# Kernel optimization log

Hardware: AMD Instinct MI355X
Metric: run time of the kernel (lower is better)

The kernel has to match this reference:

```python
import jax, jax.numpy as jnp
import numpy as np

BLOCK = 32          # MX block size along the last (contraction) dim
E4M3_MAX = 448.0    # max representable magnitude of float8_e4m3fn
E4M3_MAX_POW2 = 8.0 # floor(log2(448))


def mx_quant_dequant(x):
    """Emulate torchao MXTensor.to_mx: per-32-block shared E8M0 scale + fp8 e4m3 cast,
    then dequantize back to fp32 (what torch.matmul on MXTensor computes with)."""
    orig_shape = x.shape
    xb = x.reshape(orig_shape[:-1] + (orig_shape[-1] // BLOCK, BLOCK))
    amax = jnp.max(jnp.abs(xb), axis=-1, keepdims=True)
    safe_amax = jnp.where(amax == 0, 1.0, amax)
    # shared power-of-two exponent: floor(log2(amax)) - max_pow2(e4m3)
    shared_exp = jnp.floor(jnp.log2(safe_amax)) - E4M3_MAX_POW2
    scale = jnp.exp2(jnp.clip(shared_exp, -127.0, 127.0))  # E8M0 range
    q = jnp.clip(xb / scale, -E4M3_MAX, E4M3_MAX).astype(jnp.float8_e4m3fn)
    return (q.astype(x.dtype) * scale).reshape(orig_shape)


def setup_inputs() -> dict:
    key = jax.random.key(0)
    k1, k2, k3 = jax.random.split(key, 3)
    M = K = N = 4096
    return {
        "x_mx": jax.random.normal(k1, (M, K), dtype=jnp.float32),
        "mat1": jax.random.normal(k2, (K, K), dtype=jnp.float32),
        "mat2": jax.random.normal(k3, (K, N), dtype=jnp.float32),
    }


def reference(x_mx, mat1, mat2):
    # inputs arrive as MX tensors in the original -> quantize/dequantize them first
    xq = mx_quant_dequant(x_mx)
    m1q = mx_quant_dequant(mat1)
    m2q = mx_quant_dequant(mat2)
    x_high = xq @ m1q                       # [M, K] fp32 matmul of dequantized MX
    x_requant = mx_quant_dequant(x_high)    # re-quantize intermediate to MX fp8
    out = x_requant @ m2q                   # [M, N]
    return out
```

## Files before the change

### kernel.cpp

```cpp
#include <hip/hip_runtime.h>
#include <cstdint>

typedef unsigned short u16;
typedef __bf16 bf16x8 __attribute__((ext_vector_type(8)));
typedef float f32x4 __attribute__((ext_vector_type(4)));
typedef float f32x2 __attribute__((ext_vector_type(2)));

#define AS1 __attribute__((address_space(1)))
#define AS3 __attribute__((address_space(3)))


__device__ __forceinline__ int floor_log2(float x) {
    unsigned b = __float_as_uint(x);
    if (b < 0x00800000u) {
        b = __float_as_uint(x * 16777216.0f);
        return (int)(b >> 23) - 151;
    }
    return (int)(b >> 23) - 127;
}

__device__ __forceinline__ float exp2i(int e) {
    if (e >= -126) return __uint_as_float((unsigned)(e + 127) << 23);
    return __uint_as_float(0x00400000u >> (-127 - e));
}

__device__ __forceinline__ int shared_exp(float amax) {
    float safe = (amax == 0.0f) ? 1.0f : amax;
    int se = floor_log2(safe) - 8;
    return se < -127 ? -127 : (se > 127 ? 127 : se);
}

__device__ __forceinline__ void qdq2s(float v0, float v1, float i0, float i1,
                                      float s0, float s1, float& o0, float& o1) {
    float y0 = fminf(fmaxf(v0 * i0, -448.0f), 448.0f);
    float y1 = fminf(fmaxf(v1 * i1, -448.0f), 448.0f);
    int pk = __builtin_amdgcn_cvt_pk_fp8_f32(y0, y1, 0, false);
    f32x2 f = __builtin_amdgcn_cvt_pk_f32_fp8(pk, false);
    o0 = f.x * s0;
    o1 = f.y * s1;
}

__device__ __forceinline__ unsigned pack_bf16(float a, float b) {
    return (__float_as_uint(a) >> 16) | (__float_as_uint(b) & 0xffff0000u);
}


__device__ __forceinline__ void qdq_rows_body(const float* __restrict__ in,
                                              u16* __restrict__ out, int bid) {
    size_t t = (size_t)bid * 256 + threadIdx.x;
    float4 v0 = ((const float4*)in)[t * 2];
    float4 v1 = ((const float4*)in)[t * 2 + 1];
    float a = fmaxf(fmaxf(fabsf(v0.x), fabsf(v0.y)), fmaxf(fabsf(v0.z), fabsf(v0.w)));
    a = fmaxf(a, fmaxf(fmaxf(fabsf(v1.x), fabsf(v1.y)), fmaxf(fabsf(v1.z), fabsf(v1.w))));
    a = fmaxf(a, __shfl_xor(a, 1));
    a = fmaxf(a, __shfl_xor(a, 2));
    int se = shared_exp(a);
    float s = exp2i(se), inv = exp2i(-se);
    float q0, q1, q2, q3, q4, q5, q6, q7;
    qdq2s(v0.x, v0.y, inv, inv, s, s, q0, q1);
    qdq2s(v0.z, v0.w, inv, inv, s, s, q2, q3);
    qdq2s(v1.x, v1.y, inv, inv, s, s, q4, q5);
    qdq2s(v1.z, v1.w, inv, inv, s, s, q6, q7);
    uint4 o;
    o.x = pack_bf16(q0, q1);
    o.y = pack_bf16(q2, q3);
    o.z = pack_bf16(q4, q5);
    o.w = pack_bf16(q6, q7);
    ((uint4*)out)[t] = o;
}

__device__ __forceinline__ void qdq_transpose_body(const float* __restrict__ in,
                                                   u16* __restrict__ out,
                                                   int bx, int by,
                                                   u16 (*tile)[70]) {
    const int R = 4096, C = 4096;
    int c0 = bx * 64, r0 = by * 64;
    int t = threadIdx.x;
    #pragma unroll
    for (int p = 0; p < 4; ++p) {
        int lin = p * 256 + t;
        int row = lin >> 4;
        int c4  = lin & 15;
        float4 v = *(const float4*)(in + (size_t)(r0 + row) * C + c0 + c4 * 4);
        float a = fmaxf(fmaxf(fabsf(v.x), fabsf(v.y)), fmaxf(fabsf(v.z), fabsf(v.w)));
        a = fmaxf(a, __shfl_xor(a, 1));
        a = fmaxf(a, __shfl_xor(a, 2));
        a = fmaxf(a, __shfl_xor(a, 4));
        int se = shared_exp(a);
        float s = exp2i(se), inv = exp2i(-se);
        float q0, q1, q2, q3;
        qdq2s(v.x, v.y, inv, inv, s, s, q0, q1);
        qdq2s(v.z, v.w, inv, inv, s, s, q2, q3);
        tile[c4 * 4 + 0][row] = (u16)(__float_as_uint(q0) >> 16);
        tile[c4 * 4 + 1][row] = (u16)(__float_as_uint(q1) >> 16);
        tile[c4 * 4 + 2][row] = (u16)(__float_as_uint(q2) >> 16);
        tile[c4 * 4 + 3][row] = (u16)(__float_as_uint(q3) >> 16);
    }
    __syncthreads();
    #pragma unroll
    for (int p = 0; p < 4; ++p) {
        int lin = p * 256 + t;
        int n  = lin >> 4;
        int k4 = lin & 15;
        unsigned lo = *(const unsigned*)&tile[n][k4 * 4];
        unsigned hi = *(const unsigned*)&tile[n][k4 * 4 + 2];
        *(uint2*)(out + (size_t)(c0 + n) * R + r0 + k4 * 4) = make_uint2(lo, hi);
    }
}

__global__ void qdq_all(const float* __restrict__ x,  u16* __restrict__ xq,
                        const float* __restrict__ m1, u16* __restrict__ m1qT,
                        const float* __restrict__ m2, u16* __restrict__ m2qT) {
    __shared__ u16 tile[64][70];
    int bid = blockIdx.x;
    if (bid < 8192) {
        qdq_rows_body(x, xq, bid);
    } else if (bid < 12288) {
        int j = bid - 8192;
        qdq_transpose_body(m1, m1qT, j & 63, j >> 6, tile);
    } else {
        int j = bid - 12288;
        qdq_transpose_body(m2, m2qT, j & 63, j >> 6, tile);
    }
}

__device__ __forceinline__ void gemm_core256(const u16* __restrict__ A,
                                             const u16* __restrict__ B,
                                             u16* As, u16* Bs,
                                             int m0, int n0, f32x4 acc[8][4]) {
    const int K = 4096;
    const int t = threadIdx.x;
    const int w = t >> 6, lane = t & 63;
    const int l15 = lane & 15, lq = lane >> 4, fr = l15 & 7;
    const int wmc = (w >> 2) * 64;
    const int wnc = (w & 3) * 32;

    int aofs[2], bofs[2];
    #pragma unroll
    for (int ks = 0; ks < 2; ++ks) {
        aofs[ks] = (wmc + l15) * 64 + (((ks * 4 + lq) ^ fr) * 8);
        bofs[ks] = (wnc + l15) * 64 + (((ks * 4 + lq) ^ fr) * 8);
    }

    const int ch0 = t, ch1 = 512 + t;
    const int r0 = ch0 >> 3, r1 = ch1 >> 3;
    const size_t soff0 = (size_t)r0 * K + ((ch0 & 7) ^ (r0 & 7)) * 8;
    const size_t soff1 = (size_t)r1 * K + ((ch1 & 7) ^ (r1 & 7)) * 8;
    const int doff0 = ch0 * 8, doff1 = ch1 * 8;

    const u16* pA0 = A + (size_t)m0 * K;
    const u16* pA1 = A + (size_t)(m0 + 128) * K;
    const u16* pB0 = B + (size_t)n0 * K;
    const u16* pB1 = B + (size_t)(n0 + 128) * K;

    u16* A0b0 = As;            u16* A1b0 = As + 8192;
    u16* A0b1 = As + 16384;    u16* A1b1 = As + 24576;
    u16* B0b0 = Bs;            u16* B1b0 = Bs + 8192;
    u16* B0b1 = Bs + 16384;    u16* B1b1 = Bs + 24576;

#define STAGE(dst, src, kt) do {                                                          \
    __builtin_amdgcn_global_load_lds((const AS1 unsigned*)((src) + soff0 + (size_t)(kt) * 64), \
                                     (AS3 unsigned*)&(dst)[doff0], 16, 0, 0);             \
    __builtin_amdgcn_global_load_lds((const AS1 unsigned*)((src) + soff1 + (size_t)(kt) * 64), \
                                     (AS3 unsigned*)&(dst)[doff1], 16, 0, 0); } while (0)

#define LOAD_A(dst, base) do {                                                            \
    _Pragma("unroll") for (int m = 0; m < 4; ++m)                                         \
    _Pragma("unroll") for (int ks = 0; ks < 2; ++ks)                                      \
        dst[m][ks] = *(const bf16x8*)&(base)[aofs[ks] + m * 1024]; } while (0)

#define LOAD_B(dst, base) do {                                                            \
    _Pragma("unroll") for (int nf = 0; nf < 2; ++nf)                                      \
    _Pragma("unroll") for (int ks = 0; ks < 2; ++ks)                                      \
        dst[nf][ks] = *(const bf16x8*)&(base)[bofs[ks] + nf * 1024]; } while (0)

#define MFMA_Q(mb, nb, AF, BF) do {                                                       \
    _Pragma("unroll") for (int ks = 0; ks < 2; ++ks)                                      \
    _Pragma("unroll") for (int m = 0; m < 4; ++m)                                         \
    _Pragma("unroll") for (int nf = 0; nf < 2; ++nf)                                      \
        acc[(mb) + m][(nb) + nf] = __builtin_amdgcn_mfma_f32_16x16x32_bf16(               \
            AF[m][ks], BF[nf][ks], acc[(mb) + m][(nb) + nf], 0, 0, 0); } while (0)

#define MID() do { __builtin_amdgcn_s_barrier();                                          \
    asm volatile("s_waitcnt lgkmcnt(0)" ::: "memory");                                    \
    __builtin_amdgcn_s_setprio(1); } while (0)
#define END() do { __builtin_amdgcn_s_setprio(0); __builtin_amdgcn_s_barrier(); } while (0)
#define VMW() asm volatile("s_waitcnt vmcnt(6)" ::: "memory")

    #pragma unroll
    for (int mi = 0; mi < 8; ++mi)
        #pragma unroll
        for (int ni = 0; ni < 4; ++ni)
            acc[mi][ni] = (f32x4)0.f;

    bf16x8 afA[4][2], afB[4][2], bf0[2][2], bf1[2][2];

    STAGE(A0b0, pA0, 0);
    STAGE(B1b0, pB1, 0);
    STAGE(A1b0, pA1, 0);
    STAGE(B0b0, pB0, 0);
    STAGE(A0b1, pA0, 1);
    STAGE(B1b1, pB1, 1);
    STAGE(A1b1, pA1, 1);
    VMW();
    __builtin_amdgcn_s_barrier();
    LOAD_A(afA, A0b0); LOAD_B(bf0, B0b0);

    #pragma unroll 1
    for (int i = 0; i < 32; ++i) {
        const int t1 = (2 * i + 1) & 63, t2 = (2 * i + 2) & 63, t3 = (2 * i + 3) & 63;
        STAGE(B0b1, pB0, t1);
        MID(); LOAD_B(bf1, B1b0); MFMA_Q(0, 0, afA, bf0); END();
        STAGE(A0b0, pA0, t2);
        MID(); LOAD_A(afB, A1b0); MFMA_Q(0, 2, afA, bf1); END();
        STAGE(B1b0, pB1, t2);
        MID(); MFMA_Q(4, 2, afB, bf1); END();
        STAGE(A1b0, pA1, t2);
        VMW();
        MID(); LOAD_A(afA, A0b1); LOAD_B(bf1, B0b1); MFMA_Q(4, 0, afB, bf0); END();
        STAGE(B0b0, pB0, t2);
        MID(); LOAD_B(bf0, B1b1); MFMA_Q(0, 0, afA, bf1); END();
        STAGE(A0b1, pA0, t3);
        MID(); LOAD_A(afB, A1b1); MFMA_Q(0, 2, afA, bf0); END();
        STAGE(B1b1, pB1, t3);
        MID(); MFMA_Q(4, 2, afB, bf0); END();
        STAGE(A1b1, pA1, t3);
        VMW();
        MID(); LOAD_A(afA, A0b0); LOAD_B(bf0, B0b0); MFMA_Q(4, 0, afB, bf1); END();
    }
#undef STAGE
#undef LOAD_A
#undef LOAD_B
#undef MFMA_Q
#undef MID
#undef END
#undef VMW
}

__device__ __forceinline__ void swizzle_bid(int& m0, int& n0) {
    int id = blockIdx.x;
    int wg = (id & 7) * 32 + (id >> 3);
    m0 = (wg >> 4) * 256;
    n0 = (wg & 15) * 256;
}

__global__ __launch_bounds__(512, 2) void gemm1_fused(const u16* __restrict__ A,
                                                      const u16* __restrict__ B,
                                                      u16* __restrict__ Cq) {
    const int N = 4096;
    extern __shared__ __align__(16) char smem[];
    u16* As = (u16*)smem;
    u16* Bs = (u16*)(smem + 65536);
    int m0, n0;
    swizzle_bid(m0, n0);
    f32x4 acc[8][4];
    gemm_core256(A, B, As, Bs, m0, n0, acc);

    const int t = threadIdx.x, w = t >> 6, lane = t & 63;
    const int l15 = lane & 15, lq = lane >> 4;
    const int wmc = (w >> 2) * 64, wnc = (w & 3) * 32;

    #pragma unroll
    for (int mi = 0; mi < 8; ++mi) {
        const int gr_base = m0 + (mi >> 2) * 128 + wmc + (mi & 3) * 16 + lq * 4;
        #pragma unroll
        for (int nq = 0; nq < 2; ++nq) {
            const int gc = n0 + nq * 128 + wnc + l15;
            float sc[4], iv[4];
            #pragma unroll
            for (int reg = 0; reg < 4; ++reg) {
                float a = fmaxf(fabsf(acc[mi][2 * nq][reg]), fabsf(acc[mi][2 * nq + 1][reg]));
                a = fmaxf(a, __shfl_xor(a, 1));
                a = fmaxf(a, __shfl_xor(a, 2));
                a = fmaxf(a, __shfl_xor(a, 4));
                a = fmaxf(a, __shfl_xor(a, 8));
                int se = shared_exp(a);
                sc[reg] = exp2i(se);
                iv[reg] = exp2i(-se);
            }
            #pragma unroll
            for (int reg = 0; reg < 4; ++reg) {
                float q0, q1;
                qdq2s(acc[mi][2 * nq][reg], acc[mi][2 * nq + 1][reg],
                      iv[reg], iv[reg], sc[reg], sc[reg], q0, q1);
                Cq[(size_t)(gr_base + reg) * N + gc]      = (u16)(__float_as_uint(q0) >> 16);
                Cq[(size_t)(gr_base + reg) * N + gc + 16] = (u16)(__float_as_uint(q1) >> 16);
            }
        }
    }
}

__global__ __launch_bounds__(512, 2) void gemm2(const u16* __restrict__ A,
                                                const u16* __restrict__ B,
                                                float* __restrict__ C) {
    const int N = 4096;
    extern __shared__ __align__(16) char smem[];
    u16* As = (u16*)smem;
    u16* Bs = (u16*)(smem + 65536);
    int m0, n0;
    swizzle_bid(m0, n0);
    f32x4 acc[8][4];
    gemm_core256(A, B, As, Bs, m0, n0, acc);

    const int t = threadIdx.x, w = t >> 6, lane = t & 63;
    const int l15 = lane & 15, lq = lane >> 4;
    const int wmc = (w >> 2) * 64, wnc = (w & 3) * 32;

    #pragma unroll
    for (int mi = 0; mi < 8; ++mi) {
        const int gr_base = m0 + (mi >> 2) * 128 + wmc + (mi & 3) * 16 + lq * 4;
        #pragma unroll
        for (int ni = 0; ni < 4; ++ni) {
            const int gc = n0 + (ni >> 1) * 128 + wnc + (ni & 1) * 16 + l15;
            #pragma unroll
            for (int reg = 0; reg < 4; ++reg)
                C[(size_t)(gr_base + reg) * N + gc] = acc[mi][ni][reg];
        }
    }
}

extern "C" void kernel_launch(void* const* d_in, const int* in_sizes, int n_in,
                              void* d_out, int out_size, void* d_ws, size_t ws_size,
                              hipStream_t stream) {
    const float* x  = (const float*)d_in[0];
    const float* m1 = (const float*)d_in[1];
    const float* m2 = (const float*)d_in[2];
    float* out = (float*)d_out;

    const size_t MB = 1024 * 1024;
    char* ws = (char*)d_ws;
    u16* xq   = (u16*)(ws + 0 * MB);
    u16* m1qT = (u16*)(ws + 32 * MB);
    u16* m2qT = (u16*)(ws + 64 * MB);
    u16* xrq  = (u16*)(ws + 96 * MB);

    static bool s_init = false;
    if (!s_init) {
        hipFuncSetAttribute((const void*)gemm1_fused,
                            hipFuncAttributeMaxDynamicSharedMemorySize, 131072);
        hipFuncSetAttribute((const void*)gemm2,
                            hipFuncAttributeMaxDynamicSharedMemorySize, 131072);
        s_init = true;
    }

    qdq_all<<<dim3(16384), dim3(256), 0, stream>>>(x, xq, m1, m1qT, m2, m2qT);
    gemm1_fused<<<dim3(256), dim3(512), 131072, stream>>>(xq, m1qT, xrq);
    gemm2<<<dim3(256), dim3(512), 131072, stream>>>(xrq, m2qT, out);
}
```

Baseline: 411.3 us.

## Restructure GEMM main loop: drop trailing barriers, reorder staging and waits

Reworks the software-pipelined GEMM main loop. Each phase now has a single barrier instead of two, since the END barrier is removed and priority is raised only around the MFMA block. Global-to-LDS staging is reordered so all eight buffers are prefetched up front and refilled right after their consumers. The vmcnt wait threshold is relaxed from 6 to 8. The goal is to cut barrier overhead and keep more loads in flight, at the risk of LDS write-after-read hazards if the remaining barrier and wait placement does not fully order buffer reuse.

```diff
diff --git a/kernel.cpp b/kernel.cpp
--- a/kernel.cpp
+++ b/kernel.cpp
@@ -182,10 +182,10 @@
             AF[m][ks], BF[nf][ks], acc[(mb) + m][(nb) + nf], 0, 0, 0); } while (0)
 
 #define MID() do { __builtin_amdgcn_s_barrier();                                          \
-    asm volatile("s_waitcnt lgkmcnt(0)" ::: "memory");                                    \
-    __builtin_amdgcn_s_setprio(1); } while (0)
-#define END() do { __builtin_amdgcn_s_setprio(0); __builtin_amdgcn_s_barrier(); } while (0)
-#define VMW() asm volatile("s_waitcnt vmcnt(6)" ::: "memory")
+    asm volatile("s_waitcnt lgkmcnt(0)" ::: "memory"); } while (0)
+#define P1() __builtin_amdgcn_s_setprio(1)
+#define P0() __builtin_amdgcn_s_setprio(0)
+#define VMW() asm volatile("s_waitcnt vmcnt(8)" ::: "memory")
 
     #pragma unroll
     for (int mi = 0; mi < 8; ++mi)
@@ -193,47 +193,53 @@
         for (int ni = 0; ni < 4; ++ni)
             acc[mi][ni] = (f32x4)0.f;
 
-    bf16x8 afA[4][2], afB[4][2], bf0[2][2], bf1[2][2];
-
-    STAGE(A0b0, pA0, 0);
-    STAGE(B1b0, pB1, 0);
-    STAGE(A1b0, pA1, 0);
-    STAGE(B0b0, pB0, 0);
-    STAGE(A0b1, pA0, 1);
-    STAGE(B1b1, pB1, 1);
-    STAGE(A1b1, pA1, 1);
+    bf16x8 afA[4][2], afB[4][2], bfU[2][2], bfV[2][2];
+
+    STAGE(A0b0, pA0, 0); STAGE(B0b0, pB0, 0); STAGE(B1b0, pB1, 0); STAGE(A1b0, pA1, 0);
+    STAGE(A0b1, pA0, 1); STAGE(B0b1, pB0, 1); STAGE(B1b1, pB1, 1); STAGE(A1b1, pA1, 1);
     VMW();
     __builtin_amdgcn_s_barrier();
-    LOAD_A(afA, A0b0); LOAD_B(bf0, B0b0);
+    LOAD_A(afA, A0b0); LOAD_B(bfU, B0b0);
 
     #pragma unroll 1
     for (int i = 0; i < 32; ++i) {
-        const int t1 = (2 * i + 1) & 63, t2 = (2 * i + 2) & 63, t3 = (2 * i + 3) & 63;
-        STAGE(B0b1, pB0, t1);
-        MID(); LOAD_B(bf1, B1b0); MFMA_Q(0, 0, afA, bf0); END();
-        STAGE(A0b0, pA0, t2);
-        MID(); LOAD_A(afB, A1b0); MFMA_Q(0, 2, afA, bf1); END();
-        STAGE(B1b0, pB1, t2);
-        MID(); MFMA_Q(4, 2, afB, bf1); END();
-        STAGE(A1b0, pA1, t2);
+        const int kE = (2 * i + 2) & 63, kO = (2 * i + 3) & 63;
+        MID(); LOAD_B(bfV, B1b0);
+        P1(); MFMA_Q(0, 0, afA, bfU); P0();
+        STAGE(A0b0, pA0, kE);
+        MID(); LOAD_A(afB, A1b0);
+        P1(); MFMA_Q(0, 2, afA, bfV); P0();
+        STAGE(B0b0, pB0, kE);
         VMW();
-        MID(); LOAD_A(afA, A0b1); LOAD_B(bf1, B0b1); MFMA_Q(4, 0, afB, bf0); END();
-        STAGE(B0b0, pB0, t2);
-        MID(); LOAD_B(bf0, B1b1); MFMA_Q(0, 0, afA, bf1); END();
-        STAGE(A0b1, pA0, t3);
-        MID(); LOAD_A(afB, A1b1); MFMA_Q(0, 2, afA, bf0); END();
-        STAGE(B1b1, pB1, t3);
-        MID(); MFMA_Q(4, 2, afB, bf0); END();
-        STAGE(A1b1, pA1, t3);
+        MID(); LOAD_A(afA, A0b1);
+        P1(); MFMA_Q(4, 2, afB, bfV); P0();
+        STAGE(B1b0, pB1, kE);
+        MID(); LOAD_B(bfV, B0b1);
+        P1(); MFMA_Q(4, 0, afB, bfU); P0();
+        STAGE(A1b0, pA1, kE);
         VMW();
-        MID(); LOAD_A(afA, A0b0); LOAD_B(bf0, B0b0); MFMA_Q(4, 0, afB, bf1); END();
+        MID(); LOAD_B(bfU, B1b1);
+        P1(); MFMA_Q(0, 0, afA, bfV); P0();
+        STAGE(A0b1, pA0, kO);
+        MID(); LOAD_A(afB, A1b1);
+        P1(); MFMA_Q(0, 2, afA, bfU); P0();
+        STAGE(B0b1, pB0, kO);
+        VMW();
+        MID(); LOAD_A(afA, A0b0);
+        P1(); MFMA_Q(4, 2, afB, bfU); P0();
+        STAGE(B1b1, pB1, kO);
+        MID(); LOAD_B(bfU, B0b0);
+        P1(); MFMA_Q(4, 0, afB, bfV); P0();
+        STAGE(A1b1, pA1, kO);
+        VMW();
     }
 #undef STAGE
 #undef LOAD_A
 #undef LOAD_B
 #undef MFMA_Q
 #undef MID
-#undef END
+#undef P1
+#undef P0
 #undef VMW
 }
 
```

Result: slower. 567.6 us (+38.0%).
